# Kernel optimization log

Measured on AMD Instinct MI355X. Metric: run time of the kernel, lower is better.

The kernel has to match this reference:

```python
import jax, jax.numpy as jnp
import numpy as np

V, E, H2, K = 30000, 256, 256, 13  # vocab, embed dim, per-direction hidden, num tags
B, T = 64, 512


def setup_inputs() -> dict:
    key = jax.random.key(0)
    ks = jax.random.split(key, 12)
    s = 0.1
    return {
        "x": jax.random.randint(ks[0], (B, T), 0, V, dtype=jnp.int32),
        "emb": jax.random.normal(ks[1], (V, E), dtype=jnp.float32) * s,
        "w_ih_f": jax.random.normal(ks[2], (4 * H2, E), dtype=jnp.float32) * s,
        "w_hh_f": jax.random.normal(ks[3], (4 * H2, H2), dtype=jnp.float32) * s,
        "b_ih_f": jnp.zeros((4 * H2,), jnp.float32),
        "b_hh_f": jnp.zeros((4 * H2,), jnp.float32),
        "w_ih_b": jax.random.normal(ks[4], (4 * H2, E), dtype=jnp.float32) * s,
        "w_hh_b": jax.random.normal(ks[5], (4 * H2, H2), dtype=jnp.float32) * s,
        "b_ih_b": jnp.zeros((4 * H2,), jnp.float32),
        "b_hh_b": jnp.zeros((4 * H2,), jnp.float32),
        "w_out": jax.random.normal(ks[6], (K, 2 * H2), dtype=jnp.float32) * s,
        "b_out": jnp.zeros((K,), jnp.float32),
        "start_trans": jax.random.normal(ks[7], (K,), dtype=jnp.float32) * s,
        "end_trans": jax.random.normal(ks[8], (K,), dtype=jnp.float32) * s,
        "trans": jax.random.normal(ks[9], (K, K), dtype=jnp.float32) * s,
    }


def _lstm_dir(xg, w_hh, reverse):
    # xg: [T, B, 4H] precomputed input-side gate pre-activations (PyTorch i|f|g|o order)
    Bsz, H = xg.shape[1], w_hh.shape[1]

    def step(carry, g_in):
        h, c = carry
        g = g_in + h @ w_hh.T
        i, f, gg, o = jnp.split(g, 4, axis=-1)
        c = jax.nn.sigmoid(f) * c + jax.nn.sigmoid(i) * jnp.tanh(gg)
        h = jax.nn.sigmoid(o) * jnp.tanh(c)
        return (h, c), h

    init = (jnp.zeros((Bsz, H), xg.dtype), jnp.zeros((Bsz, H), xg.dtype))
    _, hs = jax.lax.scan(step, init, xg, reverse=reverse)
    return hs  # [T, B, H]


def reference(x, emb, w_ih_f, w_hh_f, b_ih_f, b_hh_f, w_ih_b, w_hh_b, b_ih_b, b_hh_b,
              w_out, b_out, start_trans, end_trans, trans):
    e = emb[x].transpose(1, 0, 2)                     # [T, B, E] time-major
    xg_f = e @ w_ih_f.T + (b_ih_f + b_hh_f)           # [T, B, 4H] (fold both biases)
    xg_b = e @ w_ih_b.T + (b_ih_b + b_hh_b)
    h_f = _lstm_dir(xg_f, w_hh_f, reverse=False)
    h_b = _lstm_dir(xg_b, w_hh_b, reverse=True)
    h = jnp.concatenate([h_f, h_b], axis=-1)          # [T, B, 2H]; dropout = identity (eval)
    emissions = h @ w_out.T + b_out                   # [T, B, K]

    # CRF Viterbi decode (torchcrf semantics, full mask)
    score = start_trans + emissions[0]                # [B, K]

    def vstep(score, emit_t):
        s = score[:, :, None] + trans[None] + emit_t[:, None, :]  # [B, K_prev, K_next]
        return s.max(axis=1), s.argmax(axis=1)

    score, bps = jax.lax.scan(vstep, score, emissions[1:])        # bps: [T-1, B, K]
    score = score + end_trans
    best_last = jnp.argmax(score, axis=-1)            # [B]
    best_score = jnp.max(score, axis=-1)              # [B]

    def btstep(tag, bp_t):
        prev = jnp.take_along_axis(bp_t, tag[:, None], axis=1)[:, 0]
        return prev, prev

    _, path_head = jax.lax.scan(btstep, best_last, bps, reverse=True)  # [T-1, B]
    path = jnp.concatenate([path_head, best_last[None]], axis=0).T     # [B, T]
    return path, best_score
```

## Files before the change

### kernel.cpp

```cpp
#include <hip/hip_runtime.h>
#include <stdint.h>
#include <stddef.h>

#define T_LEN  512
#define BATCH  64
#define NTAG   13
#define CT     64
#define NCHUNK 8

__device__ __forceinline__ float sigm(float x) { return 1.0f / (1.0f + expf(-x)); }

__global__ __launch_bounds__(256) void xg_gemm(
    const int* __restrict__ x, const float* __restrict__ emb,
    const float* __restrict__ w_ih_f, const float* __restrict__ w_ih_b,
    const float* __restrict__ b_ih_f, const float* __restrict__ b_hh_f,
    const float* __restrict__ b_ih_b, const float* __restrict__ b_hh_b,
    float* __restrict__ xg_ws, int chunk)
{
    const int tid = threadIdx.x;
    const int mt = blockIdx.x;
    const int nt = blockIdx.y;
    const int d  = blockIdx.z;
    const int tbase = (d == 0 ? chunk : (NCHUNK - 1 - chunk)) * CT;
    const float* W  = (d == 0) ? w_ih_f : w_ih_b;
    const float* bi = (d == 0) ? b_ih_f : b_ih_b;
    const float* bh = (d == 0) ? b_hh_f : b_hh_b;

    __shared__ __align__(16) float Wl[16][132];
    __shared__ __align__(16) float El[16][132];
    __shared__ int tok[128];

    if (tid < 128) {
        int col = nt * 128 + tid;
        tok[tid] = x[(col & 63) * T_LEN + tbase + (col >> 6)];
    }
    __syncthreads();

    const int r  = tid >> 1;
    const int c8 = (tid & 1) * 8;
    const int tm = tid >> 4;
    const int tn = tid & 15;

    float acc[8][8];
#pragma unroll
    for (int i = 0; i < 8; i++)
#pragma unroll
        for (int jz = 0; jz < 8; jz++) acc[i][jz] = 0.0f;

    const float* wrow = &W[(size_t)(mt * 128 + r) * 256];
    const float* erow = &emb[(size_t)tok[r] * 256];

    for (int kb = 0; kb < 256; kb += 16) {
        float4 w0 = *(const float4*)&wrow[kb + c8];
        float4 w1 = *(const float4*)&wrow[kb + c8 + 4];
        float4 e0 = *(const float4*)&erow[kb + c8];
        float4 e1 = *(const float4*)&erow[kb + c8 + 4];
        __syncthreads();
        Wl[c8+0][r] = w0.x; Wl[c8+1][r] = w0.y; Wl[c8+2][r] = w0.z; Wl[c8+3][r] = w0.w;
        Wl[c8+4][r] = w1.x; Wl[c8+5][r] = w1.y; Wl[c8+6][r] = w1.z; Wl[c8+7][r] = w1.w;
        El[c8+0][r] = e0.x; El[c8+1][r] = e0.y; El[c8+2][r] = e0.z; El[c8+3][r] = e0.w;
        El[c8+4][r] = e1.x; El[c8+5][r] = e1.y; El[c8+6][r] = e1.z; El[c8+7][r] = e1.w;
        __syncthreads();
#pragma unroll
        for (int kk = 0; kk < 16; kk++) {
            float a[8], b[8];
            *(float4*)&a[0] = *(const float4*)&Wl[kk][tm*8];
            *(float4*)&a[4] = *(const float4*)&Wl[kk][tm*8+4];
            *(float4*)&b[0] = *(const float4*)&El[kk][tn*8];
            *(float4*)&b[4] = *(const float4*)&El[kk][tn*8+4];
#pragma unroll
            for (int i = 0; i < 8; i++)
#pragma unroll
                for (int jz = 0; jz < 8; jz++)
                    acc[i][jz] += a[i] * b[jz];
        }
    }

    const int colbase = nt * 128 + tn * 8;
    const int j  = colbase >> 6;
    const int b0 = colbase & 63;
#pragma unroll
    for (int gi = 0; gi < 8; gi++) {
        int g = mt * 128 + tm * 8 + gi;
        float bias = bi[g] + bh[g];
        float* dst = &xg_ws[(((size_t)(d * CT + j) * 1024 + g) << 6) + b0];
        float4 v0 = make_float4(acc[gi][0]+bias, acc[gi][1]+bias, acc[gi][2]+bias, acc[gi][3]+bias);
        float4 v1 = make_float4(acc[gi][4]+bias, acc[gi][5]+bias, acc[gi][6]+bias, acc[gi][7]+bias);
        *(float4*)dst       = v0;
        *(float4*)(dst + 4) = v1;
    }
}

__global__ __launch_bounds__(256) void lstm_chunk(
    const float* __restrict__ xg_ws,
    const float* __restrict__ w_hh_f, const float* __restrict__ w_hh_b,
    float* h_ex, float* c_state, float* h_all, int* flags, int chunk)
{
    const int tid = threadIdx.x;
    const int bid = blockIdx.x;
    const int dg    = bid & 7;
    const int slice = bid >> 3;
    const int dir = dg & 1;
    const int grp = dg >> 1;
    const int h_base = slice * 8;
    const int sbase  = grp * 16;

    __shared__ __align__(16) float w_lds[32][260];
    __shared__ __align__(16) float h_lds[16][260];
    __shared__ __align__(16) float red[7][32][20];
    __shared__ float gatebuf[32][17];

    const float* W = dir ? w_hh_b : w_hh_f;
    for (int idx = tid; idx < 2048; idx += 256) {
        int f  = idx << 2;
        int rr = f >> 8;
        int c4 = f & 255;
        int row = (rr >> 3) * 256 + h_base + (rr & 7);
        *(float4*)&w_lds[rr][c4] = *(const float4*)&W[(size_t)row * 256 + c4];
    }

    const int ih_g = tid & 7;
    const int s_g  = tid >> 3;
    float c_val = 0.0f;
    if (tid < 128)
        c_val = c_state[(size_t)(dir * 64 + sbase + s_g) * 256 + h_base + ih_g];

    {
        const float* base = &h_ex[((size_t)dg * 16) * 256];
#pragma unroll
        for (int i = 0; i < 8; i++) {
            int pos = tid + 256 * i;
            int fo  = pos << 1;
            unsigned long long u64 = __hip_atomic_load(
                (const unsigned long long*)(base + fo), __ATOMIC_RELAXED, __HIP_MEMORY_SCOPE_AGENT);
            float2 v = __builtin_bit_cast(float2, u64);
            *(float2*)&h_lds[fo >> 8][fo & 255] = v;
        }
    }
    __syncthreads();

    const int kc   = tid >> 5;
    const int tile = tid & 31;
    const int gt = tile >> 2;
    const int st = tile & 3;
    const float* wr[4] = { &w_lds[gt][0], &w_lds[8+gt][0], &w_lds[16+gt][0], &w_lds[24+gt][0] };
    const float* hr[4] = { &h_lds[st][0], &h_lds[4+st][0], &h_lds[8+st][0],  &h_lds[12+st][0] };

    float hv_prev = 0.0f;
    size_t ha_prev = 0;

#pragma unroll 1
    for (int tl = 0; tl < CT; tl++) {
        const int jslot = dir ? (CT - 1 - tl) : tl;
        const int t = (dir ? (NCHUNK - 1 - chunk) : chunk) * CT + jslot;
        const int sc = chunk * CT + tl + 1;
        const int par = sc & 1;

        float xg0 = 0.f, xg1 = 0.f, xg2 = 0.f, xg3 = 0.f;
        if (tid < 128) {
            if (tl > 0) h_all[ha_prev] = hv_prev;
            const float* xp = &xg_ws[(((size_t)(dir * CT + jslot) * 1024) + h_base + ih_g) * 64 + sbase + s_g];
            xg0 = xp[0];
            xg1 = xp[1 * 256 * 64];
            xg2 = xp[2 * 256 * 64];
            xg3 = xp[3 * 256 * 64];
        }

        float acc[4][4];
#pragma unroll
        for (int gi = 0; gi < 4; gi++)
#pragma unroll
            for (int si = 0; si < 4; si++) acc[gi][si] = 0.0f;

        const int j0 = kc * 32;
#pragma unroll
        for (int m = 0; m < 8; m++) {
            const int jj = j0 + m * 4;
            float4 w4[4], h4[4];
#pragma unroll
            for (int i = 0; i < 4; i++) w4[i] = *(const float4*)(wr[i] + jj);
#pragma unroll
            for (int i = 0; i < 4; i++) h4[i] = *(const float4*)(hr[i] + jj);
#pragma unroll
            for (int gi = 0; gi < 4; gi++)
#pragma unroll
                for (int si = 0; si < 4; si++)
                    acc[gi][si] += w4[gi].x*h4[si].x + w4[gi].y*h4[si].y
                                 + w4[gi].z*h4[si].z + w4[gi].w*h4[si].w;
        }

        if (kc >= 1) {
#pragma unroll
            for (int gi = 0; gi < 4; gi++)
                *(float4*)&red[kc-1][tile][gi*4] =
                    make_float4(acc[gi][0], acc[gi][1], acc[gi][2], acc[gi][3]);
        }
        __syncthreads();
        if (kc == 0) {
#pragma unroll
            for (int p = 0; p < 7; p++)
#pragma unroll
                for (int gi = 0; gi < 4; gi++) {
                    float4 v = *(const float4*)&red[p][tile][gi*4];
                    acc[gi][0] += v.x; acc[gi][1] += v.y; acc[gi][2] += v.z; acc[gi][3] += v.w;
                }
#pragma unroll
            for (int gi = 0; gi < 4; gi++)
#pragma unroll
                for (int si = 0; si < 4; si++)
                    gatebuf[8*gi + gt][4*si + st] = acc[gi][si];
        }
        __syncthreads();

        if (tid < 128) {
            float gI = gatebuf[     ih_g][s_g] + xg0;
            float gF = gatebuf[8  + ih_g][s_g] + xg1;
            float gG = gatebuf[16 + ih_g][s_g] + xg2;
            float gO = gatebuf[24 + ih_g][s_g] + xg3;
            c_val = sigm(gF) * c_val + sigm(gI) * tanhf(gG);
            float hv = sigm(gO) * tanhf(c_val);
            __hip_atomic_store(&h_ex[(((size_t)par * 8 + dg) * 16 + s_g) * 256 + h_base + ih_g],
                               hv, __ATOMIC_RELAXED, __HIP_MEMORY_SCOPE_AGENT);
            hv_prev = hv;
            ha_prev = ((size_t)t * 64 + sbase + s_g) * 512 + dir * 256 + h_base + ih_g;
        }
        __syncthreads();

        if (tid == 0)
            __hip_atomic_store(&flags[dg * 32 + slice], sc, __ATOMIC_RELAXED, __HIP_MEMORY_SCOPE_AGENT);

        if (tid < 64) {
            const int* fp = &flags[dg * 32 + (tid & 31)];
            int spins = 0;
            int v = __hip_atomic_load(fp, __ATOMIC_RELAXED, __HIP_MEMORY_SCOPE_AGENT);
            while (__ballot(v < sc) != 0ull) {
                if (++spins > 8) __builtin_amdgcn_s_sleep(1);
                v = __hip_atomic_load(fp, __ATOMIC_RELAXED, __HIP_MEMORY_SCOPE_AGENT);
                if (spins > (1 << 20)) break;
            }
        }
        __syncthreads();

        {
            const float* base = &h_ex[(((size_t)par * 8 + dg) * 16) * 256];
#pragma unroll
            for (int i = 0; i < 8; i++) {
                int pos = tid + 256 * i;
                int fo  = pos << 1;
                unsigned long long u64 = __hip_atomic_load(
                    (const unsigned long long*)(base + fo), __ATOMIC_RELAXED, __HIP_MEMORY_SCOPE_AGENT);
                float2 v = __builtin_bit_cast(float2, u64);
                *(float2*)&h_lds[fo >> 8][fo & 255] = v;
            }
        }
        __syncthreads();
    }

    if (tid < 128) {
        h_all[ha_prev] = hv_prev;
        c_state[(size_t)(dir * 64 + sbase + s_g) * 256 + h_base + ih_g] = c_val;
    }
}

__global__ __launch_bounds__(256) void emis_kernel(
    const float* __restrict__ h_all, const float* __restrict__ w_out,
    const float* __restrict__ b_out, float* __restrict__ emis)
{
    const int row = blockIdx.x * 16 + (threadIdx.x >> 4);
    const int k   = threadIdx.x & 15;
    const float* hr = &h_all[(size_t)row * 512];
    const float* wr = &w_out[(size_t)(k < NTAG ? k : 0) * 512];
    float acc = 0.0f;
#pragma unroll 8
    for (int e = 0; e < 512; e += 4) {
        float4 h4 = *(const float4*)&hr[e];
        float4 w4 = *(const float4*)&wr[e];
        acc += h4.x*w4.x + h4.y*w4.y + h4.z*w4.z + h4.w*w4.w;
    }
    if (k < NTAG) emis[(size_t)row * NTAG + k] = acc + b_out[k];
}

__global__ __launch_bounds__(64) void viterbi_kernel(
    const float* __restrict__ emis, const float* __restrict__ start_trans,
    const float* __restrict__ end_trans, const float* __restrict__ trans,
    float* __restrict__ out)
{
    const int b = blockIdx.x;
    const int k = threadIdx.x;
    __shared__ float em[T_LEN * NTAG];
    __shared__ unsigned char bp[T_LEN][16];

    for (int t = k; t < T_LEN; t += 64) {
        const float* src = &emis[((size_t)t * 64 + b) * NTAG];
#pragma unroll
        for (int kk = 0; kk < NTAG; kk++)
            em[t * NTAG + kk] = src[kk];
    }
    __syncthreads();

    float tc[NTAG];
#pragma unroll
    for (int kp = 0; kp < NTAG; kp++)
        tc[kp] = (k < NTAG) ? trans[kp * NTAG + k] : 0.0f;

    float score = (k < NTAG) ? (start_trans[k] + em[k]) : -3.0e38f;

    for (int t = 1; t < T_LEN; t++) {
        float best = -3.0e38f;
        int bi = 0;
#pragma unroll
        for (int kp = 0; kp < NTAG; kp++) {
            float v = __shfl(score, kp) + tc[kp];
            if (v > best) { best = v; bi = kp; }
        }
        if (k < NTAG) {
            score = best + em[t * NTAG + k];
            bp[t][k] = (unsigned char)bi;
        }
    }
    if (k < NTAG) score += end_trans[k];
    else score = -3.0e38f;
    __syncthreads();

    float bs = -3.0e38f;
    int tag = 0;
#pragma unroll
    for (int kk = 0; kk < NTAG; kk++) {
        float v = __shfl(score, kk);
        if (v > bs) { bs = v; tag = kk; }
    }
    if (k == 0) {
        out[32768 + b] = bs;
        int tg = tag;
        out[b * T_LEN + (T_LEN - 1)] = (float)tg;
        for (int t = T_LEN - 1; t >= 1; t--) {
            tg = bp[t][tg];
            out[b * T_LEN + t - 1] = (float)tg;
        }
    }
}

extern "C" void kernel_launch(void* const* d_in, const int* in_sizes, int n_in,
                              void* d_out, int out_size, void* d_ws, size_t ws_size,
                              hipStream_t stream)
{
    (void)in_sizes; (void)n_in; (void)out_size; (void)ws_size;
    const int*   x    = (const int*)  d_in[0];
    const float* emb  = (const float*)d_in[1];
    const float* wihf = (const float*)d_in[2];
    const float* whhf = (const float*)d_in[3];
    const float* bihf = (const float*)d_in[4];
    const float* bhhf = (const float*)d_in[5];
    const float* wihb = (const float*)d_in[6];
    const float* whhb = (const float*)d_in[7];
    const float* bihb = (const float*)d_in[8];
    const float* bhhb = (const float*)d_in[9];
    const float* wout = (const float*)d_in[10];
    const float* bout = (const float*)d_in[11];
    const float* stt  = (const float*)d_in[12];
    const float* ent  = (const float*)d_in[13];
    const float* trn  = (const float*)d_in[14];
    float* out = (float*)d_out;

    char* ws = (char*)d_ws;
    size_t off = 0;
    float* xg_ws = (float*)(ws + off); off += (size_t)2 * CT * 1024 * 64 * 4;
    float* h_all = (float*)(ws + off); off += (size_t)T_LEN * 64 * 512 * 4;
    float* h_ex  = (float*)(ws + off); off += (size_t)2 * 8 * 16 * 256 * 4;
    float* c_st  = (float*)(ws + off); off += (size_t)2 * 64 * 256 * 4;
    float* emis  = (float*)(ws + off); off += (size_t)T_LEN * 64 * NTAG * 4;
    int*   flags = (int*)  (ws + off); off += 8 * 32 * 4;

    hipMemsetAsync(h_ex,  0, (size_t)2 * 8 * 16 * 256 * 4, stream);
    hipMemsetAsync(c_st,  0, (size_t)2 * 64 * 256 * 4, stream);
    hipMemsetAsync(flags, 0, 8 * 32 * 4, stream);

    for (int c = 0; c < NCHUNK; c++) {
        xg_gemm<<<dim3(8, 32, 2), 256, 0, stream>>>(x, emb, wihf, wihb,
                                                    bihf, bhhf, bihb, bhhb, xg_ws, c);
        lstm_chunk<<<256, 256, 0, stream>>>(xg_ws, whhf, whhb, h_ex, c_st, h_all, flags, c);
    }
    emis_kernel<<<2048, 256, 0, stream>>>(h_all, wout, bout, emis);
    viterbi_kernel<<<64, 64, 0, stream>>>(emis, stt, ent, trn, out);
}
```

Before: 3.461 ms.

## Overlap next-chunk input GEMM with LSTM recurrence in a fused persistent launch

Merges the per-chunk xg GEMM and LSTM recurrence into one 768-block launch. Blocks 0-255 run the recurrence at raised priority, and the extra blocks compute the next chunk's input-gate pre-activations concurrently. Because only one xg buffer exists, the GEMM blocks poll the LSTM flags before writing each time slot, so the in-place overwrite happens only after consumption. This removes the serial GEMM launch between chunks. The risks are interference with the latency-critical spin-synchronised recurrence and a deadlock if the 256 LSTM blocks are not all co-resident.

```diff
diff --git a/kernel.cpp b/kernel.cpp
--- a/kernel.cpp
+++ b/kernel.cpp
@@ -9,6 +9,20 @@
 #define NCHUNK 8
 
 __device__ __forceinline__ float sigm(float x) { return 1.0f / (1.0f + expf(-x)); }
+
+union __align__(16) SharedU {
+    struct {
+        float w[32][260];
+        float h[16][260];
+        float red[7][32][20];
+        float gate[32][17];
+    } l;
+    struct {
+        float Wl[16][132];
+        float El[16][132];
+        int   tok[128];
+    } g;
+};
 
 __global__ __launch_bounds__(256) void xg_gemm(
     const int* __restrict__ x, const float* __restrict__ emb,
@@ -91,158 +105,46 @@
     }
 }
 
-__global__ __launch_bounds__(256) void lstm_chunk(
-    const float* __restrict__ xg_ws,
+__global__ __launch_bounds__(256) void fused_chunk(
+    const float* __restrict__ xg_ws_c, float* __restrict__ xg_ws_w,
     const float* __restrict__ w_hh_f, const float* __restrict__ w_hh_b,
-    float* h_ex, float* c_state, float* h_all, int* flags, int chunk)
+    float* h_ex, float* c_state, float* h_all, int* flags,
+    const int* __restrict__ x, const float* __restrict__ emb,
+    const float* __restrict__ w_ih_f, const float* __restrict__ w_ih_b,
+    const float* __restrict__ b_ih_f, const float* __restrict__ b_hh_f,
+    const float* __restrict__ b_ih_b, const float* __restrict__ b_hh_b,
+    int chunk)
 {
+    __shared__ SharedU smem;
     const int tid = threadIdx.x;
     const int bid = blockIdx.x;
-    const int dg    = bid & 7;
-    const int slice = bid >> 3;
-    const int dir = dg & 1;
-    const int grp = dg >> 1;
-    const int h_base = slice * 8;
-    const int sbase  = grp * 16;
-
-    __shared__ __align__(16) float w_lds[32][260];
-    __shared__ __align__(16) float h_lds[16][260];
-    __shared__ __align__(16) float red[7][32][20];
-    __shared__ float gatebuf[32][17];
-
-    const float* W = dir ? w_hh_b : w_hh_f;
-    for (int idx = tid; idx < 2048; idx += 256) {
-        int f  = idx << 2;
-        int rr = f >> 8;
-        int c4 = f & 255;
-        int row = (rr >> 3) * 256 + h_base + (rr & 7);
-        *(float4*)&w_lds[rr][c4] = *(const float4*)&W[(size_t)row * 256 + c4];
-    }
-
-    const int ih_g = tid & 7;
-    const int s_g  = tid >> 3;
-    float c_val = 0.0f;
-    if (tid < 128)
-        c_val = c_state[(size_t)(dir * 64 + sbase + s_g) * 256 + h_base + ih_g];
-
-    {
-        const float* base = &h_ex[((size_t)dg * 16) * 256];
-#pragma unroll
-        for (int i = 0; i < 8; i++) {
-            int pos = tid + 256 * i;
-            int fo  = pos << 1;
-            unsigned long long u64 = __hip_atomic_load(
-                (const unsigned long long*)(base + fo), __ATOMIC_RELAXED, __HIP_MEMORY_SCOPE_AGENT);
-            float2 v = __builtin_bit_cast(float2, u64);
-            *(float2*)&h_lds[fo >> 8][fo & 255] = v;
-        }
-    }
-    __syncthreads();
-
-    const int kc   = tid >> 5;
-    const int tile = tid & 31;
-    const int gt = tile >> 2;
-    const int st = tile & 3;
-    const float* wr[4] = { &w_lds[gt][0], &w_lds[8+gt][0], &w_lds[16+gt][0], &w_lds[24+gt][0] };
-    const float* hr[4] = { &h_lds[st][0], &h_lds[4+st][0], &h_lds[8+st][0],  &h_lds[12+st][0] };
-
-    float hv_prev = 0.0f;
-    size_t ha_prev = 0;
-
-#pragma unroll 1
-    for (int tl = 0; tl < CT; tl++) {
-        const int jslot = dir ? (CT - 1 - tl) : tl;
-        const int t = (dir ? (NCHUNK - 1 - chunk) : chunk) * CT + jslot;
-        const int sc = chunk * CT + tl + 1;
-        const int par = sc & 1;
-
-        float xg0 = 0.f, xg1 = 0.f, xg2 = 0.f, xg3 = 0.f;
-        if (tid < 128) {
-            if (tl > 0) h_all[ha_prev] = hv_prev;
-            const float* xp = &xg_ws[(((size_t)(dir * CT + jslot) * 1024) + h_base + ih_g) * 64 + sbase + s_g];
-            xg0 = xp[0];
-            xg1 = xp[1 * 256 * 64];
-            xg2 = xp[2 * 256 * 64];
-            xg3 = xp[3 * 256 * 64];
-        }
-
-        float acc[4][4];
-#pragma unroll
-        for (int gi = 0; gi < 4; gi++)
-#pragma unroll
-            for (int si = 0; si < 4; si++) acc[gi][si] = 0.0f;
-
-        const int j0 = kc * 32;
-#pragma unroll
-        for (int m = 0; m < 8; m++) {
-            const int jj = j0 + m * 4;
-            float4 w4[4], h4[4];
-#pragma unroll
-            for (int i = 0; i < 4; i++) w4[i] = *(const float4*)(wr[i] + jj);
-#pragma unroll
-            for (int i = 0; i < 4; i++) h4[i] = *(const float4*)(hr[i] + jj);
-#pragma unroll
-            for (int gi = 0; gi < 4; gi++)
-#pragma unroll
-                for (int si = 0; si < 4; si++)
-                    acc[gi][si] += w4[gi].x*h4[si].x + w4[gi].y*h4[si].y
-                                 + w4[gi].z*h4[si].z + w4[gi].w*h4[si].w;
-        }
-
-        if (kc >= 1) {
-#pragma unroll
-            for (int gi = 0; gi < 4; gi++)
-                *(float4*)&red[kc-1][tile][gi*4] =
-                    make_float4(acc[gi][0], acc[gi][1], acc[gi][2], acc[gi][3]);
-        }
-        __syncthreads();
-        if (kc == 0) {
-#pragma unroll
-            for (int p = 0; p < 7; p++)
-#pragma unroll
-                for (int gi = 0; gi < 4; gi++) {
-                    float4 v = *(const float4*)&red[p][tile][gi*4];
-                    acc[gi][0] += v.x; acc[gi][1] += v.y; acc[gi][2] += v.z; acc[gi][3] += v.w;
-                }
-#pragma unroll
-            for (int gi = 0; gi < 4; gi++)
-#pragma unroll
-                for (int si = 0; si < 4; si++)
-                    gatebuf[8*gi + gt][4*si + st] = acc[gi][si];
-        }
-        __syncthreads();
-
-        if (tid < 128) {
-            float gI = gatebuf[     ih_g][s_g] + xg0;
-            float gF = gatebuf[8  + ih_g][s_g] + xg1;
-            float gG = gatebuf[16 + ih_g][s_g] + xg2;
-            float gO = gatebuf[24 + ih_g][s_g] + xg3;
-            c_val = sigm(gF) * c_val + sigm(gI) * tanhf(gG);
-            float hv = sigm(gO) * tanhf(c_val);
-            __hip_atomic_store(&h_ex[(((size_t)par * 8 + dg) * 16 + s_g) * 256 + h_base + ih_g],
-                               hv, __ATOMIC_RELAXED, __HIP_MEMORY_SCOPE_AGENT);
-            hv_prev = hv;
-            ha_prev = ((size_t)t * 64 + sbase + s_g) * 512 + dir * 256 + h_base + ih_g;
-        }
-        __syncthreads();
-
-        if (tid == 0)
-            __hip_atomic_store(&flags[dg * 32 + slice], sc, __ATOMIC_RELAXED, __HIP_MEMORY_SCOPE_AGENT);
-
-        if (tid < 64) {
-            const int* fp = &flags[dg * 32 + (tid & 31)];
-            int spins = 0;
-            int v = __hip_atomic_load(fp, __ATOMIC_RELAXED, __HIP_MEMORY_SCOPE_AGENT);
-            while (__ballot(v < sc) != 0ull) {
-                if (++spins > 8) __builtin_amdgcn_s_sleep(1);
-                v = __hip_atomic_load(fp, __ATOMIC_RELAXED, __HIP_MEMORY_SCOPE_AGENT);
-                if (spins > (1 << 20)) break;
-            }
-        }
-        __syncthreads();
+
+    if (bid < 256) {
+        __builtin_amdgcn_s_setprio(3);
+        const int dg    = bid & 7;
+        const int slice = bid >> 3;
+        const int dir = dg & 1;
+        const int grp = dg >> 1;
+        const int h_base = slice * 8;
+        const int sbase  = grp * 16;
+
+        const float* W = dir ? w_hh_b : w_hh_f;
+        for (int idx = tid; idx < 2048; idx += 256) {
+            int f  = idx << 2;
+            int rr = f >> 8;
+            int c4 = f & 255;
+            int row = (rr >> 3) * 256 + h_base + (rr & 7);
+            *(float4*)&smem.l.w[rr][c4] = *(const float4*)&W[(size_t)row * 256 + c4];
+        }
+
+        const int ih_g = tid & 7;
+        const int s_g  = tid >> 3;
+        float c_val = 0.0f;
+        if (tid < 128)
+            c_val = c_state[(size_t)(dir * 64 + sbase + s_g) * 256 + h_base + ih_g];
 
         {
-            const float* base = &h_ex[(((size_t)par * 8 + dg) * 16) * 256];
+            const float* base = &h_ex[((size_t)dg * 16) * 256];
 #pragma unroll
             for (int i = 0; i < 8; i++) {
                 int pos = tid + 256 * i;
@@ -250,15 +152,222 @@
                 unsigned long long u64 = __hip_atomic_load(
                     (const unsigned long long*)(base + fo), __ATOMIC_RELAXED, __HIP_MEMORY_SCOPE_AGENT);
                 float2 v = __builtin_bit_cast(float2, u64);
-                *(float2*)&h_lds[fo >> 8][fo & 255] = v;
+                *(float2*)&smem.l.h[fo >> 8][fo & 255] = v;
             }
         }
         __syncthreads();
-    }
-
-    if (tid < 128) {
-        h_all[ha_prev] = hv_prev;
-        c_state[(size_t)(dir * 64 + sbase + s_g) * 256 + h_base + ih_g] = c_val;
+
+        const int kc   = tid >> 5;
+        const int tile = tid & 31;
+        const int gt = tile >> 2;
+        const int st = tile & 3;
+        const float* wr[4] = { &smem.l.w[gt][0], &smem.l.w[8+gt][0], &smem.l.w[16+gt][0], &smem.l.w[24+gt][0] };
+        const float* hr[4] = { &smem.l.h[st][0], &smem.l.h[4+st][0], &smem.l.h[8+st][0],  &smem.l.h[12+st][0] };
+
+        float hv_prev = 0.0f;
+        size_t ha_prev = 0;
+
+#pragma unroll 1
+        for (int tl = 0; tl < CT; tl++) {
+            const int jslot = dir ? (CT - 1 - tl) : tl;
+            const int t = (dir ? (NCHUNK - 1 - chunk) : chunk) * CT + jslot;
+            const int sc = chunk * CT + tl + 1;
+            const int par = sc & 1;
+
+            float xg0 = 0.f, xg1 = 0.f, xg2 = 0.f, xg3 = 0.f;
+            if (tid < 128) {
+                if (tl > 0) h_all[ha_prev] = hv_prev;
+                const float* xp = &xg_ws_c[(((size_t)(dir * CT + jslot) * 1024) + h_base + ih_g) * 64 + sbase + s_g];
+                xg0 = xp[0];
+                xg1 = xp[1 * 256 * 64];
+                xg2 = xp[2 * 256 * 64];
+                xg3 = xp[3 * 256 * 64];
+            }
+
+            float acc[4][4];
+#pragma unroll
+            for (int gi = 0; gi < 4; gi++)
+#pragma unroll
+                for (int si = 0; si < 4; si++) acc[gi][si] = 0.0f;
+
+            const int j0 = kc * 32;
+#pragma unroll
+            for (int m = 0; m < 8; m++) {
+                const int jj = j0 + m * 4;
+                float4 w4[4], h4[4];
+#pragma unroll
+                for (int i = 0; i < 4; i++) w4[i] = *(const float4*)(wr[i] + jj);
+#pragma unroll
+                for (int i = 0; i < 4; i++) h4[i] = *(const float4*)(hr[i] + jj);
+#pragma unroll
+                for (int gi = 0; gi < 4; gi++)
+#pragma unroll
+                    for (int si = 0; si < 4; si++)
+                        acc[gi][si] += w4[gi].x*h4[si].x + w4[gi].y*h4[si].y
+                                     + w4[gi].z*h4[si].z + w4[gi].w*h4[si].w;
+            }
+
+            if (kc >= 1) {
+#pragma unroll
+                for (int gi = 0; gi < 4; gi++)
+                    *(float4*)&smem.l.red[kc-1][tile][gi*4] =
+                        make_float4(acc[gi][0], acc[gi][1], acc[gi][2], acc[gi][3]);
+            }
+            __syncthreads();
+            if (kc == 0) {
+#pragma unroll
+                for (int p = 0; p < 7; p++)
+#pragma unroll
+                    for (int gi = 0; gi < 4; gi++) {
+                        float4 v = *(const float4*)&smem.l.red[p][tile][gi*4];
+                        acc[gi][0] += v.x; acc[gi][1] += v.y; acc[gi][2] += v.z; acc[gi][3] += v.w;
+                    }
+#pragma unroll
+                for (int gi = 0; gi < 4; gi++)
+#pragma unroll
+                    for (int si = 0; si < 4; si++)
+                        smem.l.gate[8*gi + gt][4*si + st] = acc[gi][si];
+            }
+            __syncthreads();
+
+            if (tid < 128) {
+                float gI = smem.l.gate[     ih_g][s_g] + xg0;
+                float gF = smem.l.gate[8  + ih_g][s_g] + xg1;
+                float gG = smem.l.gate[16 + ih_g][s_g] + xg2;
+                float gO = smem.l.gate[24 + ih_g][s_g] + xg3;
+                c_val = sigm(gF) * c_val + sigm(gI) * tanhf(gG);
+                float hv = sigm(gO) * tanhf(c_val);
+                __hip_atomic_store(&h_ex[(((size_t)par * 8 + dg) * 16 + s_g) * 256 + h_base + ih_g],
+                                   hv, __ATOMIC_RELAXED, __HIP_MEMORY_SCOPE_AGENT);
+                hv_prev = hv;
+                ha_prev = ((size_t)t * 64 + sbase + s_g) * 512 + dir * 256 + h_base + ih_g;
+            }
+            __syncthreads();
+
+            if (tid == 0)
+                __hip_atomic_store(&flags[dg * 32 + slice], sc, __ATOMIC_RELAXED, __HIP_MEMORY_SCOPE_AGENT);
+
+            if (tid < 64) {
+                const int* fp = &flags[dg * 32 + (tid & 31)];
+                int spins = 0;
+                int v = __hip_atomic_load(fp, __ATOMIC_RELAXED, __HIP_MEMORY_SCOPE_AGENT);
+                while (__ballot(v < sc) != 0ull) {
+                    if (++spins > 8) __builtin_amdgcn_s_sleep(1);
+                    v = __hip_atomic_load(fp, __ATOMIC_RELAXED, __HIP_MEMORY_SCOPE_AGENT);
+                    if (spins > (1 << 20)) break;
+                }
+            }
+            __syncthreads();
+
+            {
+                const float* base = &h_ex[(((size_t)par * 8 + dg) * 16) * 256];
+#pragma unroll
+                for (int i = 0; i < 8; i++) {
+                    int pos = tid + 256 * i;
+                    int fo  = pos << 1;
+                    unsigned long long u64 = __hip_atomic_load(
+                        (const unsigned long long*)(base + fo), __ATOMIC_RELAXED, __HIP_MEMORY_SCOPE_AGENT);
+                    float2 v = __builtin_bit_cast(float2, u64);
+                    *(float2*)&smem.l.h[fo >> 8][fo & 255] = v;
+                }
+            }
+            __syncthreads();
+        }
+
+        if (tid < 128) {
+            h_all[ha_prev] = hv_prev;
+            c_state[(size_t)(dir * 64 + sbase + s_g) * 256 + h_base + ih_g] = c_val;
+        }
+    } else {
+        if (chunk == NCHUNK - 1) return;
+        const int v  = bid - 256;
+        const int mt = v & 7;
+        const int nt = (v >> 3) & 31;
+        const int d  = v >> 8;
+        const int cn = chunk + 1;
+        const int tbase = (d == 0 ? cn : (NCHUNK - 1 - cn)) * CT;
+        const float* W  = (d == 0) ? w_ih_f : w_ih_b;
+        const float* bi = (d == 0) ? b_ih_f : b_ih_b;
+        const float* bh = (d == 0) ? b_hh_f : b_hh_b;
+
+        if (tid < 128) {
+            int col = nt * 128 + tid;
+            smem.g.tok[tid] = x[(col & 63) * T_LEN + tbase + (col >> 6)];
+        }
+        __syncthreads();
+
+        const int r  = tid >> 1;
+        const int c8 = (tid & 1) * 8;
+        const int tm = tid >> 4;
+        const int tn = tid & 15;
+
+        float acc[8][8];
+#pragma unroll
+        for (int i = 0; i < 8; i++)
+#pragma unroll
+            for (int jz = 0; jz < 8; jz++) acc[i][jz] = 0.0f;
+
+        const float* wrow = &W[(size_t)(mt * 128 + r) * 256];
+        const float* erow = &emb[(size_t)smem.g.tok[r] * 256];
+
+        for (int kb = 0; kb < 256; kb += 16) {
+            float4 w0 = *(const float4*)&wrow[kb + c8];
+            float4 w1 = *(const float4*)&wrow[kb + c8 + 4];
+            float4 e0 = *(const float4*)&erow[kb + c8];
+            float4 e1 = *(const float4*)&erow[kb + c8 + 4];
+            __syncthreads();
+            smem.g.Wl[c8+0][r] = w0.x; smem.g.Wl[c8+1][r] = w0.y; smem.g.Wl[c8+2][r] = w0.z; smem.g.Wl[c8+3][r] = w0.w;
+            smem.g.Wl[c8+4][r] = w1.x; smem.g.Wl[c8+5][r] = w1.y; smem.g.Wl[c8+6][r] = w1.z; smem.g.Wl[c8+7][r] = w1.w;
+            smem.g.El[c8+0][r] = e0.x; smem.g.El[c8+1][r] = e0.y; smem.g.El[c8+2][r] = e0.z; smem.g.El[c8+3][r] = e0.w;
+            smem.g.El[c8+4][r] = e1.x; smem.g.El[c8+5][r] = e1.y; smem.g.El[c8+6][r] = e1.z; smem.g.El[c8+7][r] = e1.w;
+            __syncthreads();
+#pragma unroll
+            for (int kk = 0; kk < 16; kk++) {
+                float a[8], b[8];
+                *(float4*)&a[0] = *(const float4*)&smem.g.Wl[kk][tm*8];
+                *(float4*)&a[4] = *(const float4*)&smem.g.Wl[kk][tm*8+4];
+                *(float4*)&b[0] = *(const float4*)&smem.g.El[kk][tn*8];
+                *(float4*)&b[4] = *(const float4*)&smem.g.El[kk][tn*8+4];
+#pragma unroll
+                for (int i = 0; i < 8; i++)
+#pragma unroll
+                    for (int jz = 0; jz < 8; jz++)
+                        acc[i][jz] += a[i] * b[jz];
+            }
+        }
+
+        {
+            const int target = (d == 0) ? (chunk * CT + 2 * nt + 2)
+                                        : (chunk * CT + CT - 2 * nt);
+            if (tid < 64) {
+                const int l = tid;
+                const int* f0 = &flags[(d + 2 * (l >> 5)) * 32 + (l & 31)];
+                const int* f1 = &flags[(d + 2 * ((l >> 5) + 2)) * 32 + (l & 31)];
+                int spins = 0;
+                for (;;) {
+                    int a0 = __hip_atomic_load(f0, __ATOMIC_RELAXED, __HIP_MEMORY_SCOPE_AGENT);
+                    int a1 = __hip_atomic_load(f1, __ATOMIC_RELAXED, __HIP_MEMORY_SCOPE_AGENT);
+                    if (__ballot(a0 < target || a1 < target) == 0ull) break;
+                    __builtin_amdgcn_s_sleep(8);
+                    if (++spins > (1 << 20)) break;
+                }
+            }
+            __syncthreads();
+        }
+
+        const int colbase = nt * 128 + tn * 8;
+        const int j  = colbase >> 6;
+        const int b0 = colbase & 63;
+#pragma unroll
+        for (int gi = 0; gi < 8; gi++) {
+            int g = mt * 128 + tm * 8 + gi;
+            float bias = bi[g] + bh[g];
+            float* dst = &xg_ws_w[(((size_t)(d * CT + j) * 1024 + g) << 6) + b0];
+            float4 v0 = make_float4(acc[gi][0]+bias, acc[gi][1]+bias, acc[gi][2]+bias, acc[gi][3]+bias);
+            float4 v1 = make_float4(acc[gi][4]+bias, acc[gi][5]+bias, acc[gi][6]+bias, acc[gi][7]+bias);
+            *(float4*)dst       = v0;
+            *(float4*)(dst + 4) = v1;
+        }
     }
 }
 
@@ -375,10 +484,13 @@
     hipMemsetAsync(c_st,  0, (size_t)2 * 64 * 256 * 4, stream);
     hipMemsetAsync(flags, 0, 8 * 32 * 4, stream);
 
+    xg_gemm<<<dim3(8, 32, 2), 256, 0, stream>>>(x, emb, wihf, wihb,
+                                                bihf, bhhf, bihb, bhhb, xg_ws, 0);
     for (int c = 0; c < NCHUNK; c++) {
-        xg_gemm<<<dim3(8, 32, 2), 256, 0, stream>>>(x, emb, wihf, wihb,
-                                                    bihf, bhhf, bihb, bhhb, xg_ws, c);
-        lstm_chunk<<<256, 256, 0, stream>>>(xg_ws, whhf, whhb, h_ex, c_st, h_all, flags, c);
+        fused_chunk<<<768, 256, 0, stream>>>(xg_ws, xg_ws, whhf, whhb,
+                                             h_ex, c_st, h_all, flags,
+                                             x, emb, wihf, wihb,
+                                             bihf, bhhf, bihb, bhhb, c);
     }
     emis_kernel<<<2048, 256, 0, stream>>>(h_all, wout, bout, emis);
     viterbi_kernel<<<64, 64, 0, stream>>>(emis, stt, ent, trn, out);
```

Result: slower. 3.586 ms (+3.6%).

## Replace LDS cross-wave gate reduction with intra-wave shuffle reduction in LSTM step

Applied to the files above, without the earlier changes.

Threads are remapped so that each wave owns whole output tiles, with the 8-way K split held across lanes of the same wave. The partial gate sums are then reduced with xor-shuffles instead of an LDS `red`/`gatebuf` round trip. This removes two block-wide barriers per timestep, and every wave now polls the inter-block flags itself, which drops one more barrier. The cost is 48 shuffles per step, more threads spinning on global flags, and a larger spin count before sleeping.

```diff
diff --git a/kernel.cpp b/kernel.cpp
--- a/kernel.cpp
+++ b/kernel.cpp
@@ -107,8 +107,6 @@
 
     __shared__ __align__(16) float w_lds[32][260];
     __shared__ __align__(16) float h_lds[16][260];
-    __shared__ __align__(16) float red[7][32][20];
-    __shared__ float gatebuf[32][17];
 
     const float* W = dir ? w_hh_b : w_hh_f;
     for (int idx = tid; idx < 2048; idx += 256) {
@@ -119,11 +117,18 @@
         *(float4*)&w_lds[rr][c4] = *(const float4*)&W[(size_t)row * 256 + c4];
     }
 
-    const int ih_g = tid & 7;
-    const int s_g  = tid >> 3;
+    const int l  = tid & 63;
+    const int wv = tid >> 6;
+    const int kc   = l >> 3;
+    const int tile = wv * 8 + (l & 7);
+    const int gt = tile >> 2;
+    const int st = tile & 3;
+    const bool owner = (kc < 4);
+    const int s_loc  = st + 4 * (kc & 3);
+
     float c_val = 0.0f;
-    if (tid < 128)
-        c_val = c_state[(size_t)(dir * 64 + sbase + s_g) * 256 + h_base + ih_g];
+    if (owner)
+        c_val = c_state[(size_t)(dir * 64 + sbase + s_loc) * 256 + h_base + gt];
 
     {
         const float* base = &h_ex[((size_t)dg * 16) * 256];
@@ -139,10 +144,6 @@
     }
     __syncthreads();
 
-    const int kc   = tid >> 5;
-    const int tile = tid & 31;
-    const int gt = tile >> 2;
-    const int st = tile & 3;
     const float* wr[4] = { &w_lds[gt][0], &w_lds[8+gt][0], &w_lds[16+gt][0], &w_lds[24+gt][0] };
     const float* hr[4] = { &h_lds[st][0], &h_lds[4+st][0], &h_lds[8+st][0],  &h_lds[12+st][0] };
 
@@ -157,9 +158,9 @@
         const int par = sc & 1;
 
         float xg0 = 0.f, xg1 = 0.f, xg2 = 0.f, xg3 = 0.f;
-        if (tid < 128) {
+        if (owner) {
             if (tl > 0) h_all[ha_prev] = hv_prev;
-            const float* xp = &xg_ws[(((size_t)(dir * CT + jslot) * 1024) + h_base + ih_g) * 64 + sbase + s_g];
+            const float* xp = &xg_ws[(((size_t)(dir * CT + jslot) * 1024) + h_base + gt) * 64 + sbase + s_loc];
             xg0 = xp[0];
             xg1 = xp[1 * 256 * 64];
             xg2 = xp[2 * 256 * 64];
@@ -189,57 +190,51 @@
                                  + w4[gi].z*h4[si].z + w4[gi].w*h4[si].w;
         }
 
-        if (kc >= 1) {
-#pragma unroll
-            for (int gi = 0; gi < 4; gi++)
-                *(float4*)&red[kc-1][tile][gi*4] =
-                    make_float4(acc[gi][0], acc[gi][1], acc[gi][2], acc[gi][3]);
-        }
-        __syncthreads();
-        if (kc == 0) {
-#pragma unroll
-            for (int p = 0; p < 7; p++)
-#pragma unroll
-                for (int gi = 0; gi < 4; gi++) {
-                    float4 v = *(const float4*)&red[p][tile][gi*4];
-                    acc[gi][0] += v.x; acc[gi][1] += v.y; acc[gi][2] += v.z; acc[gi][3] += v.w;
-                }
-#pragma unroll
-            for (int gi = 0; gi < 4; gi++)
-#pragma unroll
-                for (int si = 0; si < 4; si++)
-                    gatebuf[8*gi + gt][4*si + st] = acc[gi][si];
-        }
-        __syncthreads();
-
-        if (tid < 128) {
-            float gI = gatebuf[     ih_g][s_g] + xg0;
-            float gF = gatebuf[8  + ih_g][s_g] + xg1;
-            float gG = gatebuf[16 + ih_g][s_g] + xg2;
-            float gO = gatebuf[24 + ih_g][s_g] + xg3;
+#pragma unroll
+        for (int gi = 0; gi < 4; gi++)
+#pragma unroll
+            for (int si = 0; si < 4; si++) {
+                float v = acc[gi][si];
+                v += __shfl_xor(v, 8, 64);
+                v += __shfl_xor(v, 16, 64);
+                v += __shfl_xor(v, 32, 64);
+                acc[gi][si] = v;
+            }
+
+        if (owner) {
+            float gsel[4];
+#pragma unroll
+            for (int gi = 0; gi < 4; gi++) {
+                float v01 = (kc & 1) ? acc[gi][1] : acc[gi][0];
+                float v23 = (kc & 1) ? acc[gi][3] : acc[gi][2];
+                gsel[gi] = (kc & 2) ? v23 : v01;
+            }
+            float gI = gsel[0] + xg0;
+            float gF = gsel[1] + xg1;
+            float gG = gsel[2] + xg2;
+            float gO = gsel[3] + xg3;
             c_val = sigm(gF) * c_val + sigm(gI) * tanhf(gG);
             float hv = sigm(gO) * tanhf(c_val);
-            __hip_atomic_store(&h_ex[(((size_t)par * 8 + dg) * 16 + s_g) * 256 + h_base + ih_g],
+            __hip_atomic_store(&h_ex[(((size_t)par * 8 + dg) * 16 + s_loc) * 256 + h_base + gt],
                                hv, __ATOMIC_RELAXED, __HIP_MEMORY_SCOPE_AGENT);
             hv_prev = hv;
-            ha_prev = ((size_t)t * 64 + sbase + s_g) * 512 + dir * 256 + h_base + ih_g;
+            ha_prev = ((size_t)t * 64 + sbase + s_loc) * 512 + dir * 256 + h_base + gt;
         }
         __syncthreads();
 
         if (tid == 0)
             __hip_atomic_store(&flags[dg * 32 + slice], sc, __ATOMIC_RELAXED, __HIP_MEMORY_SCOPE_AGENT);
 
-        if (tid < 64) {
-            const int* fp = &flags[dg * 32 + (tid & 31)];
+        {
+            const int* fp = &flags[dg * 32 + (l & 31)];
             int spins = 0;
             int v = __hip_atomic_load(fp, __ATOMIC_RELAXED, __HIP_MEMORY_SCOPE_AGENT);
             while (__ballot(v < sc) != 0ull) {
-                if (++spins > 8) __builtin_amdgcn_s_sleep(1);
+                if (++spins > 16) __builtin_amdgcn_s_sleep(1);
                 v = __hip_atomic_load(fp, __ATOMIC_RELAXED, __HIP_MEMORY_SCOPE_AGENT);
                 if (spins > (1 << 20)) break;
             }
         }
-        __syncthreads();
 
         {
             const float* base = &h_ex[(((size_t)par * 8 + dg) * 16) * 256];
@@ -256,9 +251,9 @@
         __syncthreads();
     }
 
-    if (tid < 128) {
+    if (owner) {
         h_all[ha_prev] = hv_prev;
-        c_state[(size_t)(dir * 64 + sbase + s_g) * 256 + h_base + ih_g] = c_val;
+        c_state[(size_t)(dir * 64 + sbase + s_loc) * 256 + h_base + gt] = c_val;
     }
 }
 
```

After: 4.278 ms. 1.24x slower.

## Tag h exchange values with step counters and keep recurrent weights in registers

Applied to the files above, without the earlier changes.

Each h value is now packed with its step number into a 64-bit word, so consumers spin on the data itself. This replaces the separate flag array, the extra barrier and the ballot-based wait. The recurrent weight tile also moves from LDS into per-thread registers (128 floats), which cuts LDS reads in the inner matvec. The cost is double-sized exchange traffic, heavy register pressure (launch_bounds min blocks 1), and per-element spinning by every thread.

```diff
diff --git a/kernel.cpp b/kernel.cpp
--- a/kernel.cpp
+++ b/kernel.cpp
@@ -91,10 +91,10 @@
     }
 }
 
-__global__ __launch_bounds__(256) void lstm_chunk(
+__global__ __launch_bounds__(256, 1) void lstm_chunk(
     const float* __restrict__ xg_ws,
     const float* __restrict__ w_hh_f, const float* __restrict__ w_hh_b,
-    float* h_ex, float* c_state, float* h_all, int* flags, int chunk)
+    unsigned long long* h_ex, float* c_state, float* h_all, int chunk)
 {
     const int tid = threadIdx.x;
     const int bid = blockIdx.x;
@@ -105,18 +105,23 @@
     const int h_base = slice * 8;
     const int sbase  = grp * 16;
 
-    __shared__ __align__(16) float w_lds[32][260];
     __shared__ __align__(16) float h_lds[16][260];
     __shared__ __align__(16) float red[7][32][20];
     __shared__ float gatebuf[32][17];
 
+    const int kc   = tid >> 5;
+    const int tile = tid & 31;
+    const int gt = tile >> 2;
+    const int st = tile & 3;
+
     const float* W = dir ? w_hh_b : w_hh_f;
-    for (int idx = tid; idx < 2048; idx += 256) {
-        int f  = idx << 2;
-        int rr = f >> 8;
-        int c4 = f & 255;
-        int row = (rr >> 3) * 256 + h_base + (rr & 7);
-        *(float4*)&w_lds[rr][c4] = *(const float4*)&W[(size_t)row * 256 + c4];
+    float4 wreg[4][8];
+#pragma unroll
+    for (int gi = 0; gi < 4; gi++) {
+        const float* wrow = &W[(size_t)(gi * 256 + h_base + gt) * 256 + kc * 32];
+#pragma unroll
+        for (int m = 0; m < 8; m++)
+            wreg[gi][m] = *(const float4*)&wrow[m * 4];
     }
 
     const int ih_g = tid & 7;
@@ -126,25 +131,20 @@
         c_val = c_state[(size_t)(dir * 64 + sbase + s_g) * 256 + h_base + ih_g];
 
     {
-        const float* base = &h_ex[((size_t)dg * 16) * 256];
-#pragma unroll
-        for (int i = 0; i < 8; i++) {
-            int pos = tid + 256 * i;
-            int fo  = pos << 1;
-            unsigned long long u64 = __hip_atomic_load(
-                (const unsigned long long*)(base + fo), __ATOMIC_RELAXED, __HIP_MEMORY_SCOPE_AGENT);
-            float2 v = __builtin_bit_cast(float2, u64);
-            *(float2*)&h_lds[fo >> 8][fo & 255] = v;
+        const unsigned long long* base = &h_ex[((size_t)dg * 16) * 256];
+        unsigned long long u[16];
+#pragma unroll
+        for (int i = 0; i < 16; i++)
+            u[i] = __hip_atomic_load(&base[tid + 256 * i], __ATOMIC_RELAXED, __HIP_MEMORY_SCOPE_AGENT);
+#pragma unroll
+        for (int i = 0; i < 16; i++) {
+            int idx = tid + 256 * i;
+            h_lds[idx >> 8][idx & 255] = __builtin_bit_cast(float, (unsigned int)u[i]);
         }
     }
     __syncthreads();
 
-    const int kc   = tid >> 5;
-    const int tile = tid & 31;
-    const int gt = tile >> 2;
-    const int st = tile & 3;
-    const float* wr[4] = { &w_lds[gt][0], &w_lds[8+gt][0], &w_lds[16+gt][0], &w_lds[24+gt][0] };
-    const float* hr[4] = { &h_lds[st][0], &h_lds[4+st][0], &h_lds[8+st][0],  &h_lds[12+st][0] };
+    const float* hr[4] = { &h_lds[st][0], &h_lds[4+st][0], &h_lds[8+st][0], &h_lds[12+st][0] };
 
     float hv_prev = 0.0f;
     size_t ha_prev = 0;
@@ -176,17 +176,17 @@
 #pragma unroll
         for (int m = 0; m < 8; m++) {
             const int jj = j0 + m * 4;
-            float4 w4[4], h4[4];
-#pragma unroll
-            for (int i = 0; i < 4; i++) w4[i] = *(const float4*)(wr[i] + jj);
+            float4 h4[4];
 #pragma unroll
             for (int i = 0; i < 4; i++) h4[i] = *(const float4*)(hr[i] + jj);
 #pragma unroll
-            for (int gi = 0; gi < 4; gi++)
+            for (int gi = 0; gi < 4; gi++) {
+                const float4 w4 = wreg[gi][m];
 #pragma unroll
                 for (int si = 0; si < 4; si++)
-                    acc[gi][si] += w4[gi].x*h4[si].x + w4[gi].y*h4[si].y
-                                 + w4[gi].z*h4[si].z + w4[gi].w*h4[si].w;
+                    acc[gi][si] += w4.x*h4[si].x + w4.y*h4[si].y
+                                 + w4.z*h4[si].z + w4.w*h4[si].w;
+            }
         }
 
         if (kc >= 1) {
@@ -219,38 +219,33 @@
             float gO = gatebuf[24 + ih_g][s_g] + xg3;
             c_val = sigm(gF) * c_val + sigm(gI) * tanhf(gG);
             float hv = sigm(gO) * tanhf(c_val);
+            unsigned long long pk = (unsigned long long)__builtin_bit_cast(unsigned int, hv)
+                                  | ((unsigned long long)(unsigned int)sc << 32);
             __hip_atomic_store(&h_ex[(((size_t)par * 8 + dg) * 16 + s_g) * 256 + h_base + ih_g],
-                               hv, __ATOMIC_RELAXED, __HIP_MEMORY_SCOPE_AGENT);
+                               pk, __ATOMIC_RELAXED, __HIP_MEMORY_SCOPE_AGENT);
             hv_prev = hv;
             ha_prev = ((size_t)t * 64 + sbase + s_g) * 512 + dir * 256 + h_base + ih_g;
         }
-        __syncthreads();
-
-        if (tid == 0)
-            __hip_atomic_store(&flags[dg * 32 + slice], sc, __ATOMIC_RELAXED, __HIP_MEMORY_SCOPE_AGENT);
-
-        if (tid < 64) {
-            const int* fp = &flags[dg * 32 + (tid & 31)];
-            int spins = 0;
-            int v = __hip_atomic_load(fp, __ATOMIC_RELAXED, __HIP_MEMORY_SCOPE_AGENT);
-            while (__ballot(v < sc) != 0ull) {
-                if (++spins > 8) __builtin_amdgcn_s_sleep(1);
-                v = __hip_atomic_load(fp, __ATOMIC_RELAXED, __HIP_MEMORY_SCOPE_AGENT);
-                if (spins > (1 << 20)) break;
+
+        {
+            const unsigned long long* base = &h_ex[(((size_t)par * 8 + dg) * 16) * 256];
+            unsigned long long u[16];
+#pragma unroll
+            for (int i = 0; i < 16; i++)
+                u[i] = __hip_atomic_load(&base[tid + 256 * i], __ATOMIC_RELAXED, __HIP_MEMORY_SCOPE_AGENT);
+#pragma unroll
+            for (int i = 0; i < 16; i++) {
+                int spins = 0;
+                while ((int)(unsigned int)(u[i] >> 32) < sc) {
+                    if (++spins > 4) __builtin_amdgcn_s_sleep(1);
+                    u[i] = __hip_atomic_load(&base[tid + 256 * i], __ATOMIC_RELAXED, __HIP_MEMORY_SCOPE_AGENT);
+                    if (spins > (1 << 20)) break;
+                }
             }
-        }
-        __syncthreads();
-
-        {
-            const float* base = &h_ex[(((size_t)par * 8 + dg) * 16) * 256];
-#pragma unroll
-            for (int i = 0; i < 8; i++) {
-                int pos = tid + 256 * i;
-                int fo  = pos << 1;
-                unsigned long long u64 = __hip_atomic_load(
-                    (const unsigned long long*)(base + fo), __ATOMIC_RELAXED, __HIP_MEMORY_SCOPE_AGENT);
-                float2 v = __builtin_bit_cast(float2, u64);
-                *(float2*)&h_lds[fo >> 8][fo & 255] = v;
+#pragma unroll
+            for (int i = 0; i < 16; i++) {
+                int idx = tid + 256 * i;
+                h_lds[idx >> 8][idx & 255] = __builtin_bit_cast(float, (unsigned int)u[i]);
             }
         }
         __syncthreads();
@@ -366,19 +361,18 @@
     size_t off = 0;
     float* xg_ws = (float*)(ws + off); off += (size_t)2 * CT * 1024 * 64 * 4;
     float* h_all = (float*)(ws + off); off += (size_t)T_LEN * 64 * 512 * 4;
-    float* h_ex  = (float*)(ws + off); off += (size_t)2 * 8 * 16 * 256 * 4;
+    unsigned long long* h_ex = (unsigned long long*)(ws + off);
+    off += (size_t)2 * 8 * 16 * 256 * 8;
     float* c_st  = (float*)(ws + off); off += (size_t)2 * 64 * 256 * 4;
     float* emis  = (float*)(ws + off); off += (size_t)T_LEN * 64 * NTAG * 4;
-    int*   flags = (int*)  (ws + off); off += 8 * 32 * 4;
-
-    hipMemsetAsync(h_ex,  0, (size_t)2 * 8 * 16 * 256 * 4, stream);
+
+    hipMemsetAsync(h_ex,  0, (size_t)2 * 8 * 16 * 256 * 8, stream);
     hipMemsetAsync(c_st,  0, (size_t)2 * 64 * 256 * 4, stream);
-    hipMemsetAsync(flags, 0, 8 * 32 * 4, stream);
 
     for (int c = 0; c < NCHUNK; c++) {
         xg_gemm<<<dim3(8, 32, 2), 256, 0, stream>>>(x, emb, wihf, wihb,
                                                     bihf, bhhf, bihb, bhhb, xg_ws, c);
-        lstm_chunk<<<256, 256, 0, stream>>>(xg_ws, whhf, whhb, h_ex, c_st, h_all, flags, c);
+        lstm_chunk<<<256, 256, 0, stream>>>(xg_ws, whhf, whhb, h_ex, c_st, h_all, c);
     }
     emis_kernel<<<2048, 256, 0, stream>>>(h_all, wout, bout, emis);
     viterbi_kernel<<<64, 64, 0, stream>>>(emis, stt, ent, trn, out);
```

Measured after the change: 4.944 ms. 1.43x slower.
